# Performance work log

Measured on AMD Instinct MI355X. Metric: run time of the kernel, lower is better.

Reference implementation:

```python
import jax, jax.numpy as jnp
import numpy as np
import math

D_MODEL = 1024
NUM_HEADS = 16
HEAD_DIM = D_MODEL // NUM_HEADS
EPS = 1e-6
ROPE_BASE = 10000.0


def _rope_cos_sin(seq_len, dim, dtype):
    inv_freq = 1.0 / (ROPE_BASE ** (jnp.arange(0, dim, 2, dtype=jnp.float32) / dim))
    t = jnp.arange(seq_len, dtype=jnp.float32)
    freqs = jnp.outer(t, inv_freq)                 # [s, dim/2]
    emb = jnp.concatenate([freqs, freqs], axis=-1)  # [s, dim]
    return jnp.cos(emb).astype(dtype), jnp.sin(emb).astype(dtype)


def _rotate_half(x):
    x1, x2 = jnp.split(x, 2, axis=-1)
    return jnp.concatenate([-x2, x1], axis=-1)


def setup_inputs() -> dict:
    key = jax.random.key(0)
    k1, k2, k3 = jax.random.split(key, 3)
    b, s = 2, 2048
    x = jax.random.normal(k1, (b, s, D_MODEL), dtype=jnp.float32)
    norm_w = jnp.ones((D_MODEL,), dtype=jnp.float32)
    qkv_w = jax.random.normal(k2, (3 * D_MODEL, D_MODEL), dtype=jnp.float32) * (1.0 / math.sqrt(D_MODEL))
    qkv_b = jnp.zeros((3 * D_MODEL,), dtype=jnp.float32)
    proj_w = jax.random.normal(k3, (D_MODEL, D_MODEL), dtype=jnp.float32) * (1.0 / math.sqrt(D_MODEL))
    proj_b = jnp.zeros((D_MODEL,), dtype=jnp.float32)
    return {"x": x, "norm_w": norm_w, "qkv_w": qkv_w, "qkv_b": qkv_b,
            "proj_w": proj_w, "proj_b": proj_b}


def reference(x, norm_w, qkv_w, qkv_b, proj_w, proj_b):
    b, s, d = x.shape
    # RMSNorm (pre-LN)
    xn = x * jax.lax.rsqrt(jnp.mean(x * x, axis=-1, keepdims=True) + EPS) * norm_w
    # Fused QKV
    qkv = jnp.einsum('bsd,ed->bse', xn, qkv_w) + qkv_b
    q, k, v = jnp.split(qkv, 3, axis=-1)
    # [b, h, s, hd]
    def shape(t):
        return t.reshape(b, s, NUM_HEADS, HEAD_DIM).transpose(0, 2, 1, 3)
    q, k, v = shape(q), shape(k), shape(v)
    # RoPE on head_dim
    cos, sin = _rope_cos_sin(s, HEAD_DIM, x.dtype)  # [s, hd]
    q = q * cos + _rotate_half(q) * sin
    k = k * cos + _rotate_half(k) * sin
    # Naive causal attention
    scale = 1.0 / math.sqrt(HEAD_DIM)
    scores = jnp.einsum('bhqd,bhkd->bhqk', q, k) * scale
    causal = jnp.tril(jnp.ones((s, s), dtype=bool))
    scores = jnp.where(causal, scores, -jnp.inf)
    attn = jax.nn.softmax(scores, axis=-1)
    y = jnp.einsum('bhqk,bhkd->bhqd', attn, v)
    y = y.transpose(0, 2, 1, 3).reshape(b, s, d)
    return jnp.einsum('bsd,ed->bse', y, proj_w) + proj_b
```

## Files before the change

### kernel.cpp

```cpp
#include <hip/hip_runtime.h>
#include <cstdint>
#include <cstddef>

#define NB 2
#define NS 2048
#define ND 1024
#define NH 16
#define HD 64
#define ROWS 4096
#define E3 3072

using bf16 = __bf16;
typedef __attribute__((ext_vector_type(4))) __bf16 bf16x4;
typedef __attribute__((ext_vector_type(8))) __bf16 bf16x8;
typedef __attribute__((ext_vector_type(4))) float f32x4;

__device__ __forceinline__ f32x4 mfma16(bf16x8 a, bf16x8 b, f32x4 c) {
    return __builtin_amdgcn_mfma_f32_16x16x32_bf16(a, b, c, 0, 0, 0);
}

__device__ __forceinline__ void gll16(const bf16* src, bf16* lds) {
    __builtin_amdgcn_global_load_lds(
        (const __attribute__((address_space(1))) void*)src,
        (__attribute__((address_space(3))) void*)lds, 16, 0, 0);
}

__global__ __launch_bounds__(256) void prep(const float* __restrict__ qkv_w,
                                            const float* __restrict__ proj_w,
                                            const float* __restrict__ x,
                                            const float* __restrict__ norm_w,
                                            bf16* __restrict__ wq,
                                            bf16* __restrict__ xn,
                                            float4* __restrict__ tab) {
    __shared__ float wsum[4];
    int bid = blockIdx.x;
    int tid = threadIdx.x;
    if (bid < 4096) {
        const int n1 = E3 * ND;
        int i = (bid * 256 + tid) * 4;
        const float* src = (i < n1) ? (qkv_w + i) : (proj_w + (i - n1));
        float4 v = *(const float4*)src;
        bf16x4 o;
        o[0] = (bf16)v.x; o[1] = (bf16)v.y; o[2] = (bf16)v.z; o[3] = (bf16)v.w;
        *(bf16x4*)(wq + i) = o;
    } else if (bid < 8192) {
        int row = bid - 4096;
        const float* xr = x + (size_t)row * ND;
        float4 v = ((const float4*)xr)[tid];
        float ss = v.x*v.x + v.y*v.y + v.z*v.z + v.w*v.w;
        #pragma unroll
        for (int m = 32; m >= 1; m >>= 1) ss += __shfl_xor(ss, m);
        if ((tid & 63) == 0) wsum[tid >> 6] = ss;
        __syncthreads();
        float total = wsum[0] + wsum[1] + wsum[2] + wsum[3];
        float scale = rsqrtf(total * (1.0f / ND) + 1e-6f);
        float4 wv = ((const float4*)norm_w)[tid];
        bf16x4 o;
        o[0] = (bf16)(v.x * scale * wv.x);
        o[1] = (bf16)(v.y * scale * wv.y);
        o[2] = (bf16)(v.z * scale * wv.z);
        o[3] = (bf16)(v.w * scale * wv.w);
        ((bf16x4*)(xn + (size_t)row * ND))[tid] = o;
    } else {
        int idx = (bid - 8192) * 256 + tid;
        int s = idx >> 4, j = idx & 15;
        float f0 = powf(10000.0f, -(float)j * (1.0f / 32.0f));
        float f1 = powf(10000.0f, -(float)(j + 16) * (1.0f / 32.0f));
        float sn0, c0, sn1, c1;
        sincosf((float)s * f0, &sn0, &c0);
        sincosf((float)s * f1, &sn1, &c1);
        tab[idx] = make_float4(c0, sn0, c1, sn1);
    }
}

__global__ __launch_bounds__(256) void gemm_qkv_rope(const bf16* __restrict__ A,
                                                     const bf16* __restrict__ Bm,
                                                     const float* __restrict__ bias,
                                                     const float4* __restrict__ tab,
                                                     bf16* __restrict__ Qb,
                                                     bf16* __restrict__ Kb,
                                                     bf16* __restrict__ Vf) {
    const int K = ND;
    __shared__ bf16 smem[8192];
    bf16* Asm = smem;
    bf16* Bsm = smem + 4096;
    const int tid = threadIdx.x;
    const int wave = tid >> 6, lane = tid & 63;
    const int quad = lane >> 4, l15 = lane & 15;
    const int row0 = blockIdx.x * 128, col0 = blockIdx.y * 128;
    const int wr = (wave >> 1) * 64, wc = (wave & 1) * 64;
    const int srow = lane >> 2;
    const int scol = (lane & 3) * 8;

    f32x4 acc[4][4] = {};

    for (int k0 = 0; k0 < K; k0 += 32) {
        #pragma unroll
        for (int i = 0; i < 2; ++i) {
            int r = wave * 32 + i * 16;
            gll16(A + (size_t)(row0 + r + srow) * K + k0 + scol, Asm + r * 32);
            gll16(Bm + (size_t)(col0 + r + srow) * K + k0 + scol, Bsm + r * 32);
        }
        __syncthreads();
        bf16x8 af[4], bff[4];
        #pragma unroll
        for (int t = 0; t < 4; ++t) {
            af[t]  = *(const bf16x8*)(Asm + (wr + t * 16 + l15) * 32 + quad * 8);
            bff[t] = *(const bf16x8*)(Bsm + (wc + t * 16 + l15) * 32 + quad * 8);
        }
        #pragma unroll
        for (int mt = 0; mt < 4; ++mt)
            #pragma unroll
            for (int nt = 0; nt < 4; ++nt)
                acc[mt][nt] = mfma16(af[mt], bff[nt], acc[mt][nt]);
        __syncthreads();
    }

    float bb[4];
    #pragma unroll
    for (int nt = 0; nt < 4; ++nt) bb[nt] = bias[col0 + wc + nt * 16 + l15];

    const int region = col0 >> 10;
    if (region == 2) {
        const int cv = col0 - 2048 + wc;
        const int h = cv >> 6;
        const int b = row0 >> 11;
        const int sloc = row0 & (NS - 1);
        const int kg0 = (sloc + wr) >> 5;
        bf16* vh = Vf + (size_t)(b * NH + h) * 131072;
        #pragma unroll
        for (int Gw = 0; Gw < 2; ++Gw) {
            #pragma unroll
            for (int nt = 0; nt < 4; ++nt) {
                bf16x8 vf8;
                #pragma unroll
                for (int r = 0; r < 4; ++r) {
                    vf8[r]     = (bf16)(acc[2 * Gw][nt][r] + bb[nt]);
                    vf8[4 + r] = (bf16)(acc[2 * Gw + 1][nt][r] + bb[nt]);
                }
                *(bf16x8*)(vh + ((size_t)(kg0 + Gw) * 4 + nt) * 512 + lane * 8) = vf8;
            }
        }
    } else {
        const float scale = (region == 0) ? 0.125f : 1.0f;
        bf16* Ob = (region == 0) ? Qb : Kb;
        const int h = ((col0 + wc) & 1023) >> 6;
        bf16* ep = smem + wave * 2048;
        #pragma unroll
        for (int p = 0; p < 2; ++p) {
            #pragma unroll
            for (int mtl = 0; mtl < 2; ++mtl) {
                const int mt = p * 2 + mtl;
                #pragma unroll
                for (int r = 0; r < 4; ++r) {
                    int row = row0 + wr + mt * 16 + quad * 4 + r;
                    int s = row & (NS - 1);
                    float4 cs = tab[s * 16 + l15];
                    #pragma unroll
                    for (int nt = 0; nt < 4; ++nt) {
                        float v  = acc[mt][nt][r] + bb[nt];
                        float vp = acc[mt][nt ^ 2][r] + bb[nt ^ 2];
                        float cc = (nt & 1) ? cs.z : cs.x;
                        float ss = (nt & 1) ? cs.w : cs.y;
                        float res = (nt < 2) ? (v * cc - vp * ss) : (v * cc + vp * ss);
                        ep[(mtl * 16 + quad * 4 + r) * 64 + nt * 16 + l15] = (bf16)(res * scale);
                    }
                }
            }
            asm volatile("s_waitcnt lgkmcnt(0)" ::: "memory");
            const int rowp = row0 + wr + p * 32;
            const int b = rowp >> 11;
            const int s0p = rowp & (NS - 1);
            bf16* gbase = Ob + ((size_t)(b * NH + h) * NS + s0p + (lane >> 3)) * 64 + (lane & 7) * 8;
            const bf16* lbase = ep + (lane >> 3) * 64 + (lane & 7) * 8;
            #pragma unroll
            for (int i = 0; i < 4; ++i) {
                bf16x8 v8 = *(const bf16x8*)(lbase + i * 512);
                *(bf16x8*)(gbase + (size_t)i * 512) = v8;
            }
            asm volatile("s_waitcnt lgkmcnt(0)" ::: "memory");
        }
    }
}

__global__ __launch_bounds__(256) void gemm_proj(const bf16* __restrict__ A,
                                                 const bf16* __restrict__ Bm,
                                                 const float* __restrict__ bias,
                                                 float* __restrict__ C) {
    __shared__ bf16 Asm[128 * 32];
    __shared__ bf16 Bsm[64 * 32];
    const int tid = threadIdx.x;
    const int wave = tid >> 6, lane = tid & 63;
    const int quad = lane >> 4, l15 = lane & 15;
    const int row0 = blockIdx.x * 128, col0 = blockIdx.y * 64;
    const int wr = (wave >> 1) * 64, wc = (wave & 1) * 32;
    const int srow = lane >> 2;
    const int scol = (lane & 3) * 8;

    f32x4 acc[4][2] = {};

    for (int k0 = 0; k0 < ND; k0 += 32) {
        gll16(A + (size_t)(row0 + wave * 32 + srow) * ND + k0 + scol, Asm + (wave * 32) * 32);
        gll16(A + (size_t)(row0 + wave * 32 + 16 + srow) * ND + k0 + scol, Asm + (wave * 32 + 16) * 32);
        gll16(Bm + (size_t)(col0 + wave * 16 + srow) * ND + k0 + scol, Bsm + (wave * 16) * 32);
        __syncthreads();
        bf16x8 af[4], bff[2];
        #pragma unroll
        for (int t = 0; t < 4; ++t)
            af[t] = *(const bf16x8*)(Asm + (wr + t * 16 + l15) * 32 + quad * 8);
        #pragma unroll
        for (int t = 0; t < 2; ++t)
            bff[t] = *(const bf16x8*)(Bsm + (wc + t * 16 + l15) * 32 + quad * 8);
        #pragma unroll
        for (int mt = 0; mt < 4; ++mt)
            #pragma unroll
            for (int nt = 0; nt < 2; ++nt)
                acc[mt][nt] = mfma16(af[mt], bff[nt], acc[mt][nt]);
        __syncthreads();
    }

    #pragma unroll
    for (int nt = 0; nt < 2; ++nt) {
        int col = col0 + wc + nt * 16 + l15;
        float bv = bias[col];
        #pragma unroll
        for (int mt = 0; mt < 4; ++mt) {
            int row = row0 + wr + mt * 16 + quad * 4;
            #pragma unroll
            for (int r = 0; r < 4; ++r)
                C[(size_t)(row + r) * ND + col] = acc[mt][nt][r] + bv;
        }
    }
}

__global__ __launch_bounds__(256) __attribute__((amdgpu_waves_per_eu(2, 2)))
void attn(const bf16* __restrict__ Q,
          const bf16* __restrict__ K,
          const bf16* __restrict__ Vf,
          bf16* __restrict__ Y) {
    __shared__ bf16 Ksm[2][8192];
    __shared__ bf16 Vsm[2][8192];
    int bid = blockIdx.x;
    int g = bid >> 5;
    int bh = bid & 31;
    int qt = (g < 8) ? (15 - g) : (g - 8);
    int tid = threadIdx.x;
    int wave = tid >> 6, lane = tid & 63;
    int quad = lane >> 4, l15 = lane & 15;
    int q0 = qt * 128 + wave * 32;
    const bf16* Qh = Q + (size_t)bh * NS * 64;
    const bf16* Kh = K + (size_t)bh * NS * 64;
    const float NEG_INF = -__builtin_inff();

    const int krow = wave * 8 + (lane >> 3);
    const int ksx  = (lane & 7) ^ (krow & 7);
    const bf16* sK = Kh + (size_t)krow * 64 + ksx * 8;
    const bf16* sV = Vf + (size_t)bh * 131072 + wave * 2048 + lane * 8;

    const bf16* pk0 = &Ksm[0][l15 * 64 + ((quad) ^ (l15 & 7)) * 8];
    const bf16* pk1 = &Ksm[0][l15 * 64 + ((4 + quad) ^ (l15 & 7)) * 8];
    const bf16* pvf = &Vsm[0][lane * 8];

    bf16x8 bq[2][2];
    #pragma unroll
    for (int t = 0; t < 2; ++t)
        #pragma unroll
        for (int hh = 0; hh < 2; ++hh)
            bq[t][hh] = *(const bf16x8*)(Qh + (size_t)(q0 + t * 16 + l15) * 64 + hh * 32 + quad * 8);

    f32x4 o[2][4] = {};
    float lsum[2] = {0.f, 0.f};

    auto stage = [&](int c, int par) {
        const int kb = c * 128;
        bf16* dK = &Ksm[par][wave * 512];
        bf16* dV = &Vsm[par][wave * 2048];
        #pragma unroll
        for (int i = 0; i < 4; ++i)
            gll16(sK + (size_t)(kb + i * 32) * 64, dK + i * 2048);
        #pragma unroll
        for (int nt = 0; nt < 4; ++nt)
            gll16(sV + (size_t)(kb >> 5) * 2048 + nt * 512, dV + nt * 512);
    };

    auto compute = [&](int cc, int par) {
        const int kb = cc * 128;
        const int pb = par * 8192;
        bf16x8 ak[4][4], vf[4][4];
        #pragma unroll
        for (int ksub = 0; ksub < 4; ++ksub) {
            ak[ksub][0] = *(const bf16x8*)(pk0 + pb + ksub * 2048);
            ak[ksub][1] = *(const bf16x8*)(pk1 + pb + ksub * 2048);
            ak[ksub][2] = *(const bf16x8*)(pk0 + pb + ksub * 2048 + 1024);
            ak[ksub][3] = *(const bf16x8*)(pk1 + pb + ksub * 2048 + 1024);
            vf[ksub][0] = *(const bf16x8*)(pvf + pb + ksub * 2048);
            vf[ksub][1] = *(const bf16x8*)(pvf + pb + ksub * 2048 + 512);
            vf[ksub][2] = *(const bf16x8*)(pvf + pb + ksub * 2048 + 1024);
            vf[ksub][3] = *(const bf16x8*)(pvf + pb + ksub * 2048 + 1536);
        }
        #pragma unroll
        for (int ksub = 0; ksub < 4; ++ksub) {
            const int kbs = kb + ksub * 32;
            if (kbs <= q0) {
                const bool masked = (kbs == q0);
                #pragma unroll
                for (int t = 0; t < 2; ++t) {
                    f32x4 sh0 = {}, sh1 = {};
                    sh0 = mfma16(ak[ksub][0], bq[t][0], sh0);
                    sh0 = mfma16(ak[ksub][1], bq[t][1], sh0);
                    sh1 = mfma16(ak[ksub][2], bq[t][0], sh1);
                    sh1 = mfma16(ak[ksub][3], bq[t][1], sh1);
                    if (masked) {
                        int qy = q0 + t * 16 + l15;
                        #pragma unroll
                        for (int r = 0; r < 4; ++r) {
                            if (kbs + quad * 4 + r > qy)      sh0[r] = NEG_INF;
                            if (kbs + 16 + quad * 4 + r > qy) sh1[r] = NEG_INF;
                        }
                    }
                    bf16x8 pa;
                    float ls = 0.f;
                    #pragma unroll
                    for (int j = 0; j < 4; ++j) {
                        float p0 = __expf(sh0[j]);
                        float p1 = __expf(sh1[j]);
                        ls += p0 + p1;
                        pa[j] = (bf16)p0;
                        pa[4 + j] = (bf16)p1;
                    }
                    lsum[t] += ls;
                    o[t][0] = mfma16(pa, vf[ksub][0], o[t][0]);
                    o[t][1] = mfma16(pa, vf[ksub][1], o[t][1]);
                    o[t][2] = mfma16(pa, vf[ksub][2], o[t][2]);
                    o[t][3] = mfma16(pa, vf[ksub][3], o[t][3]);
                }
            }
        }
    };

    const int ncb = qt + 1;
    stage(0, 0);
    __syncthreads();
    for (int c = 0; c < ncb; ++c) {
        const int par = c & 1;
        if (c + 1 < ncb) stage(c + 1, par ^ 1);
        compute(c, par);
        __syncthreads();
    }

    int b = bh >> 4, h = bh & 15;
    bf16* ep = &Ksm[0][wave * 2048];
    #pragma unroll
    for (int t = 0; t < 2; ++t) {
        float red = lsum[t];
        red += __shfl_xor(red, 16);
        red += __shfl_xor(red, 32);
        #pragma unroll
        for (int r = 0; r < 4; ++r) {
            float il = 1.0f / __shfl(red, quad * 4 + r);
            #pragma unroll
            for (int nt = 0; nt < 4; ++nt)
                ep[(t * 16 + quad * 4 + r) * 64 + nt * 16 + l15] = (bf16)(o[t][nt][r] * il);
        }
    }
    asm volatile("s_waitcnt lgkmcnt(0)" ::: "memory");
    bf16* gbase = Y + ((size_t)(b * NS + q0 + (lane >> 3)) << 10) + h * 64 + (lane & 7) * 8;
    const bf16* lbase = ep + (lane >> 3) * 64 + (lane & 7) * 8;
    #pragma unroll
    for (int i = 0; i < 4; ++i) {
        bf16x8 v8 = *(const bf16x8*)(lbase + i * 512);
        *(bf16x8*)(gbase + ((size_t)i * 8 << 10)) = v8;
    }
}

extern "C" void kernel_launch(void* const* d_in, const int* in_sizes, int n_in,
                              void* d_out, int out_size, void* d_ws, size_t ws_size,
                              hipStream_t stream) {
    const float* x      = (const float*)d_in[0];
    const float* norm_w = (const float*)d_in[1];
    const float* qkv_w  = (const float*)d_in[2];
    const float* qkv_b  = (const float*)d_in[3];
    const float* proj_w = (const float*)d_in[4];
    const float* proj_b = (const float*)d_in[5];
    float* out = (float*)d_out;

    char* ws = (char*)d_ws;
    size_t off = 0;
    bf16* xn    = (bf16*)(ws + off); off += (size_t)ROWS * ND * 2;
    bf16* wq    = (bf16*)(ws + off); off += (size_t)E3 * ND * 2;
    bf16* wp    = (bf16*)(ws + off); off += (size_t)ND * ND * 2;
    bf16* Qb    = (bf16*)(ws + off); off += (size_t)NB * NH * NS * HD * 2;
    bf16* Kb    = (bf16*)(ws + off); off += (size_t)NB * NH * NS * HD * 2;
    bf16* Vfrag = (bf16*)(ws + off); off += (size_t)NB * NH * HD * NS * 2;
    bf16* Y     = (bf16*)(ws + off); off += (size_t)ROWS * ND * 2;
    float4* tab = (float4*)(ws + off); off += (size_t)NS * 16 * sizeof(float4);

    prep<<<8320, 256, 0, stream>>>(qkv_w, proj_w, x, norm_w, wq, xn, tab);
    gemm_qkv_rope<<<dim3(ROWS / 128, E3 / 128), 256, 0, stream>>>(xn, wq, qkv_b, tab, Qb, Kb, Vfrag);
    attn<<<NB * NH * (NS / 128), 256, 0, stream>>>(Qb, Kb, Vfrag, Y);
    gemm_proj<<<dim3(ROWS / 128, ND / 64), 256, 0, stream>>>(Y, wp, proj_b, out);
}
```

Measured before the change: 185.8 us.

## Double-buffer LDS tiles in QKV and projection GEMMs to overlap loads

Both the QKV+RoPE GEMM and the output projection GEMM now use two LDS buffers. The next K-slice is issued with global_load_lds before the MFMAs run on the current slice, and one barrier per iteration replaces the two. The aim is to hide global-to-LDS latency behind matrix math. In exchange, LDS use per block doubles, which may reduce occupancy, and the barrier still waits for the outstanding prefetch.

```diff
diff --git a/kernel.cpp b/kernel.cpp
--- a/kernel.cpp
+++ b/kernel.cpp
@@ -81,9 +81,7 @@
                                                      bf16* __restrict__ Kb,
                                                      bf16* __restrict__ Vf) {
     const int K = ND;
-    __shared__ bf16 smem[8192];
-    bf16* Asm = smem;
-    bf16* Bsm = smem + 4096;
+    __shared__ bf16 smem[16384];
     const int tid = threadIdx.x;
     const int wave = tid >> 6, lane = tid & 63;
     const int quad = lane >> 4, l15 = lane & 15;
@@ -94,19 +92,29 @@
 
     f32x4 acc[4][4] = {};
 
-    for (int k0 = 0; k0 < K; k0 += 32) {
+    auto stage = [&](int k0, int p) {
+        bf16* Ad = smem + p * 4096;
+        bf16* Bd = smem + 8192 + p * 4096;
         #pragma unroll
         for (int i = 0; i < 2; ++i) {
             int r = wave * 32 + i * 16;
-            gll16(A + (size_t)(row0 + r + srow) * K + k0 + scol, Asm + r * 32);
-            gll16(Bm + (size_t)(col0 + r + srow) * K + k0 + scol, Bsm + r * 32);
-        }
-        __syncthreads();
+            gll16(A + (size_t)(row0 + r + srow) * K + k0 + scol, Ad + r * 32);
+            gll16(Bm + (size_t)(col0 + r + srow) * K + k0 + scol, Bd + r * 32);
+        }
+    };
+
+    stage(0, 0);
+    __syncthreads();
+    for (int k0 = 0; k0 < K; k0 += 32) {
+        const int p = (k0 >> 5) & 1;
+        if (k0 + 32 < K) stage(k0 + 32, p ^ 1);
+        const bf16* As = smem + p * 4096;
+        const bf16* Bs = smem + 8192 + p * 4096;
         bf16x8 af[4], bff[4];
         #pragma unroll
         for (int t = 0; t < 4; ++t) {
-            af[t]  = *(const bf16x8*)(Asm + (wr + t * 16 + l15) * 32 + quad * 8);
-            bff[t] = *(const bf16x8*)(Bsm + (wc + t * 16 + l15) * 32 + quad * 8);
+            af[t]  = *(const bf16x8*)(As + (wr + t * 16 + l15) * 32 + quad * 8);
+            bff[t] = *(const bf16x8*)(Bs + (wc + t * 16 + l15) * 32 + quad * 8);
         }
         #pragma unroll
         for (int mt = 0; mt < 4; ++mt)
@@ -187,8 +195,7 @@
                                                  const bf16* __restrict__ Bm,
                                                  const float* __restrict__ bias,
                                                  float* __restrict__ C) {
-    __shared__ bf16 Asm[128 * 32];
-    __shared__ bf16 Bsm[64 * 32];
+    __shared__ bf16 smem[12288];
     const int tid = threadIdx.x;
     const int wave = tid >> 6, lane = tid & 63;
     const int quad = lane >> 4, l15 = lane & 15;
@@ -199,18 +206,28 @@
 
     f32x4 acc[4][2] = {};
 
+    auto stage = [&](int k0, int p) {
+        bf16* Ad = smem + p * 4096;
+        bf16* Bd = smem + 8192 + p * 2048;
+        gll16(A + (size_t)(row0 + wave * 32 + srow) * ND + k0 + scol, Ad + (wave * 32) * 32);
+        gll16(A + (size_t)(row0 + wave * 32 + 16 + srow) * ND + k0 + scol, Ad + (wave * 32 + 16) * 32);
+        gll16(Bm + (size_t)(col0 + wave * 16 + srow) * ND + k0 + scol, Bd + (wave * 16) * 32);
+    };
+
+    stage(0, 0);
+    __syncthreads();
     for (int k0 = 0; k0 < ND; k0 += 32) {
-        gll16(A + (size_t)(row0 + wave * 32 + srow) * ND + k0 + scol, Asm + (wave * 32) * 32);
-        gll16(A + (size_t)(row0 + wave * 32 + 16 + srow) * ND + k0 + scol, Asm + (wave * 32 + 16) * 32);
-        gll16(Bm + (size_t)(col0 + wave * 16 + srow) * ND + k0 + scol, Bsm + (wave * 16) * 32);
-        __syncthreads();
+        const int p = (k0 >> 5) & 1;
+        if (k0 + 32 < ND) stage(k0 + 32, p ^ 1);
+        const bf16* As = smem + p * 4096;
+        const bf16* Bs = smem + 8192 + p * 2048;
         bf16x8 af[4], bff[2];
         #pragma unroll
         for (int t = 0; t < 4; ++t)
-            af[t] = *(const bf16x8*)(Asm + (wr + t * 16 + l15) * 32 + quad * 8);
+            af[t] = *(const bf16x8*)(As + (wr + t * 16 + l15) * 32 + quad * 8);
         #pragma unroll
         for (int t = 0; t < 2; ++t)
-            bff[t] = *(const bf16x8*)(Bsm + (wc + t * 16 + l15) * 32 + quad * 8);
+            bff[t] = *(const bf16x8*)(Bs + (wc + t * 16 + l15) * 32 + quad * 8);
         #pragma unroll
         for (int mt = 0; mt < 4; ++mt)
             #pragma unroll
```

Result: faster. 172.8 us (-7.0%).
